# Kernel optimization log

Measured on AMD Instinct MI355X. Metric: run time of the kernel, lower is better.

The kernel has to match this reference:

```python
import jax, jax.numpy as jnp
import numpy as np
import math

B, S, L, D, H, NL, FF, MAXP = 4, 200, 256, 256, 8, 2, 1024, 512
VOC, EDIM, BERT_D, LBL = 50000, 50, 768, 20
DH = D // H
NEG = -1e15


def _pe_table():
    # get_embedding(max_seq_len, hidden, rel_pos_init=0): sinusoidal over 0..2*MAXP
    half = D // 2
    freq = jnp.exp(jnp.arange(half, dtype=jnp.float32) * (-math.log(10000.0) / (half - 1)))
    pos = jnp.arange(2 * MAXP + 1, dtype=jnp.float32)[:, None] * freq[None, :]
    return jnp.concatenate([jnp.sin(pos), jnp.cos(pos)], axis=1)  # [2*MAXP+1, D]


def _ln(x, g, b, eps=1e-5):
    m = x.mean(-1, keepdims=True)
    v = jnp.mean((x - m) ** 2, -1, keepdims=True)
    return (x - m) * jax.lax.rsqrt(v + eps) * g + b


def _forward(lattice, bigrams, seq_len, lex_num, pos_s, pos_e,
             bert_embed, lat_table, big_table, Wc, bc, Wl, bl, W_fus, b_fus,
             Wq, bq, Wk, bk, Wv, bv, Wr, br, u, vb, Wo, bo,
             ln1_g, ln1_b, W1, b1, W2, b2, ln2_g, ln2_b, Wout, bout):
    raw = lat_table[lattice]                                        # [B,L,EDIM]
    big = jnp.pad(big_table[bigrams], ((0, 0), (0, L - S), (0, 0)))  # pad to lattice len
    bert = jnp.pad(bert_embed, ((0, 0), (0, L - S), (0, 0)))
    raw_char = jnp.concatenate([raw, big, bert], -1)                # [B,L,868]
    idx = jnp.arange(L)
    char_mask = idx[None, :] < seq_len[:, None]
    tot_mask = idx[None, :] < (seq_len + lex_num)[:, None]
    lex_mask = tot_mask & (~char_mask)
    # embed_char masked to char positions, embed_lex masked to lexicon positions
    x = (raw_char @ Wc + bc) * char_mask[..., None] + (raw @ Wl + bl) * lex_mask[..., None]

    # four-way relative position fusion ('ff'): relu(Linear(cat[pe_ss,pe_se,pe_es,pe_ee]))
    # computed as sum of four gathered pre-projected tables (same math, no 4D concat)
    pe = _pe_table()
    T = jnp.einsum('pe,keo->kpo', pe, W_fus.reshape(4, D, D))       # [4, 2*MAXP+1, D]
    ss = pos_s[:, :, None] - pos_s[:, None, :] + MAXP
    se = pos_s[:, :, None] - pos_e[:, None, :] + MAXP
    es = pos_e[:, :, None] - pos_s[:, None, :] + MAXP
    ee = pos_e[:, :, None] - pos_e[:, None, :] + MAXP
    rel = jax.nn.relu(T[0][ss] + T[1][se] + T[2][es] + T[3][ee] + b_fus)  # [B,L,L,D]

    scale = 1.0 / math.sqrt(DH)
    for l in range(NL):
        qh = (x @ Wq[l] + bq[l]).reshape(B, L, H, DH).transpose(0, 2, 1, 3)
        kh = (x @ Wk[l] + bk[l]).reshape(B, L, H, DH).transpose(0, 2, 1, 3)
        vh = (x @ Wv[l] + bv[l]).reshape(B, L, H, DH).transpose(0, 2, 1, 3)
        rh = (rel @ Wr[l] + br[l]).reshape(B, L, L, H, DH)
        # Transformer-XL style: A+C with content bias u, B+D with position bias v
        AC = jnp.einsum('bhqd,bhkd->bhqk', qh + u[l][None, :, None, :], kh)
        BD = jnp.einsum('bhqd,bqkhd->bhqk', qh + vb[l][None, :, None, :], rh)
        score = (AC + BD) * scale
        score = jnp.where(tot_mask[:, None, None, :], score, NEG)
        attn = jax.nn.softmax(score, -1)
        out = jnp.einsum('bhqk,bhkd->bhqd', attn, vh).transpose(0, 2, 1, 3).reshape(B, L, D)
        x = _ln(out @ Wo[l] + bo[l] + x, ln1_g[l], ln1_b[l])
        h = jax.nn.relu(x @ W1[l] + b1[l]) @ W2[l] + b2[l]
        x = _ln(h + x, ln2_g[l], ln2_b[l])
    return x[:, :S] @ Wout + bout                                   # emission logits [B,S,LBL]


def setup_inputs() -> dict:
    key = jax.random.key(0)
    ks = jax.random.split(key, 32)
    p = lambda i, sh, s=0.02: jax.random.normal(ks[i], sh, jnp.float32) * s
    inp = {}
    inp['lattice'] = jax.random.randint(ks[0], (B, L), 1, VOC)
    inp['bigrams'] = jax.random.randint(ks[1], (B, S), 1, VOC)
    inp['seq_len'] = jax.random.randint(ks[2], (B,), 150, S + 1)
    inp['lex_num'] = jax.random.randint(ks[3], (B,), 20, L - S + 1)
    s_lex = jax.random.randint(ks[4], (B, L - S), 0, 180)
    e_lex = s_lex + jax.random.randint(ks[5], (B, L - S), 1, 20)
    ar = jnp.broadcast_to(jnp.arange(S), (B, S))
    inp['pos_s'] = jnp.concatenate([ar, s_lex], 1)
    inp['pos_e'] = jnp.concatenate([ar, e_lex], 1)
    inp['target'] = jax.random.randint(ks[6], (B, S), 0, LBL)
    inp['bert_embed'] = p(7, (B, S, BERT_D), 1.0)
    inp['lat_table'] = p(8, (VOC, EDIM), 1.0)
    inp['big_table'] = p(9, (VOC, EDIM), 1.0)
    cin = 2 * EDIM + BERT_D
    inp['Wc'] = p(10, (cin, D)); inp['bc'] = jnp.zeros((D,))
    inp['Wl'] = p(11, (EDIM, D)); inp['bl'] = jnp.zeros((D,))
    inp['W_fus'] = p(12, (4 * D, D)); inp['b_fus'] = jnp.zeros((D,))
    inp['Wq'] = p(13, (NL, D, D)); inp['bq'] = jnp.zeros((NL, D))
    inp['Wk'] = p(14, (NL, D, D)); inp['bk'] = jnp.zeros((NL, D))
    inp['Wv'] = p(15, (NL, D, D)); inp['bv'] = jnp.zeros((NL, D))
    inp['Wr'] = p(16, (NL, D, D)); inp['br'] = jnp.zeros((NL, D))
    inp['u'] = p(17, (NL, H, DH)); inp['vb'] = p(18, (NL, H, DH))
    inp['Wo'] = p(19, (NL, D, D)); inp['bo'] = jnp.zeros((NL, D))
    inp['ln1_g'] = jnp.ones((NL, D)); inp['ln1_b'] = jnp.zeros((NL, D))
    inp['W1'] = p(20, (NL, D, FF)); inp['b1'] = jnp.zeros((NL, FF))
    inp['W2'] = p(21, (NL, FF, D)); inp['b2'] = jnp.zeros((NL, D))
    inp['ln2_g'] = jnp.ones((NL, D)); inp['ln2_b'] = jnp.zeros((NL, D))
    inp['Wout'] = p(22, (D, LBL)); inp['bout'] = jnp.zeros((LBL,))
    return inp


def reference(lattice, bigrams, seq_len, lex_num, pos_s, pos_e, target,
              bert_embed, lat_table, big_table, Wc, bc, Wl, bl, W_fus, b_fus,
              Wq, bq, Wk, bk, Wv, bv, Wr, br, u, vb, Wo, bo,
              ln1_g, ln1_b, W1, b1, W2, b2, ln2_g, ln2_b, Wout, bout):
    # target is consumed by the downstream CRF loss (omitted); emission logits returned
    return _forward(lattice, bigrams, seq_len, lex_num, pos_s, pos_e,
                    bert_embed, lat_table, big_table, Wc, bc, Wl, bl, W_fus, b_fus,
                    Wq, bq, Wk, bk, Wv, bv, Wr, br, u, vb, Wo, bo,
                    ln1_g, ln1_b, W1, b1, W2, b2, ln2_g, ln2_b, Wout, bout)
```

## Files before the change

kernel.cpp:

```cpp
#include <hip/hip_runtime.h>
#include <math.h>

#define NB 4
#define SS 200
#define LT 256
#define DD 256
#define NH 8
#define NLAYER 2
#define FFD 1024
#define BERTD 768
#define CIN 868
#define KG 992
#define NEGINF -1e15f

__global__ void gather_kernel(const int* __restrict__ lattice, const int* __restrict__ bigrams,
                              const int* __restrict__ seq_len, const int* __restrict__ lex_num,
                              const float* __restrict__ bert, const float* __restrict__ lat_t,
                              const float* __restrict__ big_t, float* __restrict__ G)
{
    const int row = blockIdx.x, t = threadIdx.x;
    const int b = row >> 8, l = row & 255;
    const int sl = seq_len[b], tl = sl + lex_num[b];
    const float mC = (l < sl) ? 1.f : 0.f;
    const float mL = (l >= sl && l < tl) ? 1.f : 0.f;
    const int lat = lattice[row];
    const int big = (l < SS) ? bigrams[b*SS + l] : 0;
    for (int i = t; i < KG; i += 256) {
        float v;
        if (i < 50)        v = lat_t[lat*50 + i] * mC;
        else if (i < 100)  v = (l < SS) ? big_t[big*50 + (i-50)] * mC : 0.f;
        else if (i < 868)  v = (l < SS) ? bert[(b*SS + l)*BERTD + (i-100)] * mC : 0.f;
        else if (i < 918)  v = lat_t[lat*50 + (i-868)] * mL;
        else if (i == 918) v = mC;
        else if (i == 919) v = mL;
        else               v = 0.f;
        G[row*KG + i] = v;
    }
}

__global__ void wcomb_kernel(const float* __restrict__ Wc, const float* __restrict__ bc,
                             const float* __restrict__ Wl, const float* __restrict__ bl,
                             float* __restrict__ Wcomb)
{
    const int r = blockIdx.x, t = threadIdx.x;
    float v;
    if (r < 868)      v = Wc[r*DD + t];
    else if (r < 918) v = Wl[(r-868)*DD + t];
    else if (r == 918) v = bc[t];
    else if (r == 919) v = bl[t];
    else               v = 0.f;
    Wcomb[r*DD + t] = v;
}

__global__ void build_T(const float* __restrict__ W_fus, const float* __restrict__ b_fus,
                        float* __restrict__ T)
{
    __shared__ float pe[4][256];
    const int t = threadIdx.x, k = blockIdx.y;
    const int p0 = blockIdx.x * 4;
    const float fr = expf(-(float)(t & 127) * (9.210340371976184f / 127.0f));
    #pragma unroll
    for (int i = 0; i < 4; ++i) {
        int p = p0 + i;
        float arg = (float)(p > 1024 ? 0 : p) * fr;
        pe[i][t] = (t < 128) ? sinf(arg) : cosf(arg);
    }
    __syncthreads();
    float acc[4];
    const float bias = (k == 0) ? b_fus[t] : 0.f;
    #pragma unroll
    for (int i = 0; i < 4; ++i) acc[i] = bias;
    const float* W = W_fus + k * DD * DD;
    for (int e = 0; e < DD; ++e) {
        float w = W[e*DD + t];
        #pragma unroll
        for (int i = 0; i < 4; ++i) acc[i] += pe[i][e] * w;
    }
    #pragma unroll
    for (int i = 0; i < 4; ++i) {
        int p = p0 + i;
        if (p <= 1024) T[(k*1025 + p)*DD + t] = acc[i];
    }
}

__global__ void rcc_kernel(const float* __restrict__ T, float* __restrict__ Rcc)
{
    const int p = blockIdx.x, t = threadIdx.x;
    float v = T[p*DD + t] + T[(1025 + p)*DD + t] + T[(2050 + p)*DD + t] + T[(3075 + p)*DD + t];
    Rcc[p*DD + t] = fmaxf(v, 0.f);
}

__global__ void transpose_wr(const float* __restrict__ Wr, float* __restrict__ WrT)
{
    const int j = blockIdx.x & 255, l = blockIdx.x >> 8, e = threadIdx.x;
    WrT[(l*DD + j)*DD + e] = Wr[l*DD*DD + e*DD + j];
}

__global__ void pack_qkv(const float* __restrict__ Wq, const float* __restrict__ Wk,
                         const float* __restrict__ Wv, const float* __restrict__ bq,
                         const float* __restrict__ bk, const float* __restrict__ bv,
                         float* __restrict__ Wqkv, float* __restrict__ bqkv)
{
    const int l = blockIdx.x >> 8, d = blockIdx.x & 255, t = threadIdx.x;
    Wqkv[(l*DD + d)*768 + t]       = Wq[(l*DD + d)*DD + t];
    Wqkv[(l*DD + d)*768 + 256 + t] = Wk[(l*DD + d)*DD + t];
    Wqkv[(l*DD + d)*768 + 512 + t] = Wv[(l*DD + d)*DD + t];
    if (d == 0) {
        bqkv[l*768 + t]       = bq[l*DD + t];
        bqkv[l*768 + 256 + t] = bk[l*DD + t];
        bqkv[l*768 + 512 + t] = bv[l*DD + t];
    }
}

template<int BM, int BN, bool RELU>
__global__ __launch_bounds__(256) void gemmv2(const float* __restrict__ A, const float* __restrict__ W,
                       const float* __restrict__ bias, const float* __restrict__ resid,
                       float* __restrict__ C, int M, int N, int K)
{
    static_assert(BM*8 % 256 == 0 && 8*BN % 256 == 0, "loader mapping");
    __shared__ float As[32][BM+2];
    __shared__ float Bs[32][BN+4];
    constexpr int TM = BM/16, TN = BN/16;
    const int t = threadIdx.x;
    const int row0 = blockIdx.y*BM, col0 = blockIdx.x*BN;
    const int tr = (t>>4)*TM, tc = (t&15)*TN;
    float acc[TM][TN] = {};
    for (int k0 = 0; k0 < K; k0 += 32) {
        #pragma unroll
        for (int i = 0; i < BM/32; ++i) {
            int slot = t + i*256;
            int r = slot >> 3, kq = (slot & 7)*4;
            float4 av = *(const float4*)&A[(row0+r)*K + k0 + kq];
            As[kq][r] = av.x; As[kq+1][r] = av.y; As[kq+2][r] = av.z; As[kq+3][r] = av.w;
        }
        #pragma unroll
        for (int i = 0; i < BN/32; ++i) {
            int slot = t + i*256;
            int kk = slot / (BN/4), nq = (slot % (BN/4))*4;
            *(float4*)&Bs[kk][nq] = *(const float4*)&W[(k0+kk)*N + col0 + nq];
        }
        __syncthreads();
        #pragma unroll
        for (int kk = 0; kk < 32; ++kk) {
            float a[TM], bb[TN];
            #pragma unroll
            for (int i = 0; i < TM; ++i) a[i] = As[kk][tr+i];
            #pragma unroll
            for (int j = 0; j < TN; ++j) bb[j] = Bs[kk][tc+j];
            #pragma unroll
            for (int i = 0; i < TM; ++i)
                #pragma unroll
                for (int j = 0; j < TN; ++j) acc[i][j] += a[i]*bb[j];
        }
        __syncthreads();
    }
    #pragma unroll
    for (int i = 0; i < TM; ++i) {
        const int r = row0 + tr + i, c0 = col0 + tc;
        #pragma unroll
        for (int j = 0; j < TN; ++j) {
            float v = acc[i][j] + (bias ? bias[c0+j] : 0.f);
            if (resid) v += resid[r*N + c0 + j];
            if (RELU) v = fmaxf(v, 0.f);
            acc[i][j] = v;
        }
        if constexpr (TN == 4) {
            float4 v = make_float4(acc[i][0], acc[i][1], acc[i][2], acc[i][3]);
            *(float4*)&C[r*N + c0] = v;
        } else {
            float2 v = make_float2(acc[i][0], acc[i][1]);
            *(float2*)&C[r*N + c0] = v;
        }
    }
}

__global__ __launch_bounds__(256) void qr_v2(const float* __restrict__ qkvb, const float* __restrict__ vb,
                      const float* __restrict__ WrT, float* __restrict__ qr)
{
    __shared__ float qv[4][256];
    const int t = threadIdx.x, row0 = blockIdx.x * 4;
    #pragma unroll
    for (int r = 0; r < 4; ++r) qv[r][t] = qkvb[(row0+r)*768 + t] + vb[t];
    __syncthreads();
    #pragma unroll
    for (int h = 0; h < NH; ++h) {
        float acc[4] = {0.f, 0.f, 0.f, 0.f};
        const float* wt = WrT + (h*32)*DD;
        for (int d = 0; d < 32; ++d) {
            float w = wt[d*DD + t];
            #pragma unroll
            for (int r = 0; r < 4; ++r) acc[r] += qv[r][h*32 + d] * w;
        }
        #pragma unroll
        for (int r = 0; r < 4; ++r) qr[((row0+r)*NH + h)*DD + t] = acc[r];
    }
}

__global__ __launch_bounds__(256) void attn_v2(
    const float* __restrict__ qkvb, const float* __restrict__ qr,
    const float* __restrict__ T, const float* __restrict__ Rcc,
    const int* __restrict__ pos_s, const int* __restrict__ pos_e,
    const int* __restrict__ seq_len, const int* __restrict__ lex_num,
    const float* __restrict__ u, float* __restrict__ obuf)
{
    __shared__ float relb[32][260];
    __shared__ float qrl[NH][260];
    __shared__ float qu[256];
    __shared__ float sc[NH][260];
    __shared__ float redbuf[2048];
    const int t = threadIdx.x;
    const int row = blockIdx.x;
    const int b = row >> 8, q = row & 255;
    const int totlen = seq_len[b] + lex_num[b];
    if (q >= SS && q >= totlen) {
        obuf[row*DD + t] = 0.f;
        return;
    }
    qu[t] = qkvb[row*768 + t] + u[t];
    #pragma unroll
    for (int h = 0; h < NH; ++h) qrl[h][t] = qr[(row*NH + h)*DD + t];
    const int ps_q = pos_s[row], pe_q = pos_e[row];
    const int* psb = pos_s + b*LT;
    const int* peb = pos_e + b*LT;
    const bool qchar = (q < SS);
    const int br = t >> 3, bc4 = (t & 7)*4;
    const int dk = t & 31, seg = t >> 5;

    for (int K0 = 0; K0 < totlen; K0 += 32) {
        __syncthreads();
        {
            const int kg = K0 + br;
            const int sk = psb[kg], ek = peb[kg];
            if (qchar && kg < SS) {
                const float* rp = Rcc + (ps_q - sk + 512)*DD;
                #pragma unroll
                for (int i = 0; i < 8; ++i) {
                    int e = i*32 + bc4;
                    *(float4*)&relb[br][e] = *(const float4*)&rp[e];
                }
            } else {
                const float* t0 = T + (ps_q - sk + 512)*DD;
                const float* t1 = T + (1025 + ps_q - ek + 512)*DD;
                const float* t2 = T + (2050 + pe_q - sk + 512)*DD;
                const float* t3 = T + (3075 + pe_q - ek + 512)*DD;
                #pragma unroll
                for (int i = 0; i < 8; ++i) {
                    int e = i*32 + bc4;
                    float4 a = *(const float4*)&t0[e];
                    float4 bb = *(const float4*)&t1[e];
                    float4 c = *(const float4*)&t2[e];
                    float4 d = *(const float4*)&t3[e];
                    float4 v;
                    v.x = fmaxf(a.x + bb.x + c.x + d.x, 0.f);
                    v.y = fmaxf(a.y + bb.y + c.y + d.y, 0.f);
                    v.z = fmaxf(a.z + bb.z + c.z + d.z, 0.f);
                    v.w = fmaxf(a.w + bb.w + c.w + d.w, 0.f);
                    *(float4*)&relb[br][e] = v;
                }
            }
        }
        __syncthreads();
        {
            float a[8] = {0.f,0.f,0.f,0.f,0.f,0.f,0.f,0.f};
            const int e0 = seg*32;
            #pragma unroll
            for (int e4 = 0; e4 < 8; ++e4) {
                float4 r4 = *(const float4*)&relb[dk][e0 + e4*4];
                #pragma unroll
                for (int h = 0; h < 8; ++h) {
                    float4 q4 = *(const float4*)&qrl[h][e0 + e4*4];
                    a[h] += r4.x*q4.x + r4.y*q4.y + r4.z*q4.z + r4.w*q4.w;
                }
            }
            {
                const float* kp = qkvb + (size_t)(b*LT + K0 + dk)*768 + 256 + seg*32;
                float acv = 0.f;
                #pragma unroll
                for (int d4 = 0; d4 < 8; ++d4) {
                    float4 kv = *(const float4*)&kp[d4*4];
                    float4 qv = *(const float4*)&qu[seg*32 + d4*4];
                    acv += kv.x*qv.x + kv.y*qv.y + kv.z*qv.z + kv.w*qv.w;
                }
                a[seg] += acv;
            }
            float4* rb = (float4*)&redbuf[(seg*32 + dk)*8];
            rb[0] = make_float4(a[0], a[1], a[2], a[3]);
            rb[1] = make_float4(a[4], a[5], a[6], a[7]);
        }
        __syncthreads();
        {
            const int k = t >> 3, h = t & 7;
            float s = 0.f;
            #pragma unroll
            for (int g = 0; g < 8; ++g) s += redbuf[g*256 + t];
            s *= 0.17677669529663687f;
            const int kg = K0 + k;
            if (kg >= totlen) s = NEGINF;
            sc[h][kg] = s;
        }
    }
    __syncthreads();
    {
        const int g = t >> 5, lane = t & 31;
        float vals[8];
        float m = -INFINITY;
        #pragma unroll
        for (int i = 0; i < 8; ++i) {
            int kidx = lane + 32*i;
            vals[i] = (kidx < totlen) ? sc[g][kidx] : NEGINF;
            m = fmaxf(m, vals[i]);
        }
        #pragma unroll
        for (int off = 16; off >= 1; off >>= 1) m = fmaxf(m, __shfl_xor(m, off, 32));
        float sum = 0.f;
        #pragma unroll
        for (int i = 0; i < 8; ++i) { vals[i] = expf(vals[i] - m); sum += vals[i]; }
        #pragma unroll
        for (int off = 16; off >= 1; off >>= 1) sum += __shfl_xor(sum, off, 32);
        const float inv = 1.0f / sum;
        #pragma unroll
        for (int i = 0; i < 8; ++i) sc[g][lane + 32*i] = vals[i] * inv;
    }
    __syncthreads();
    {
        const int j4 = (t & 63)*4, kr = t >> 6;
        const int h = j4 >> 5;
        float4 acc = make_float4(0.f, 0.f, 0.f, 0.f);
        const float* vp = qkvb + (size_t)(b*LT)*768 + 512 + j4;
        for (int k = kr; k < totlen; k += 4) {
            const float p = sc[h][k];
            float4 v = *(const float4*)&vp[(size_t)k*768];
            acc.x += p*v.x; acc.y += p*v.y; acc.z += p*v.z; acc.w += p*v.w;
        }
        *(float4*)&redbuf[kr*256 + j4] = acc;
    }
    __syncthreads();
    obuf[row*DD + t] = redbuf[t] + redbuf[256 + t] + redbuf[512 + t] + redbuf[768 + t];
}

__global__ void ln_kernel(const float* __restrict__ in, const float* __restrict__ g,
                          const float* __restrict__ bb, float* __restrict__ out)
{
    __shared__ float red[4];
    const int t = threadIdx.x, row = blockIdx.x;
    float v = in[row*DD + t];
    float s = v;
    #pragma unroll
    for (int off = 32; off >= 1; off >>= 1) s += __shfl_xor(s, off, 64);
    if ((t & 63) == 0) red[t >> 6] = s;
    __syncthreads();
    float m = (red[0] + red[1] + red[2] + red[3]) * (1.0f/256.0f);
    __syncthreads();
    float d = v - m;
    float s2 = d*d;
    #pragma unroll
    for (int off = 32; off >= 1; off >>= 1) s2 += __shfl_xor(s2, off, 64);
    if ((t & 63) == 0) red[t >> 6] = s2;
    __syncthreads();
    float var = (red[0] + red[1] + red[2] + red[3]) * (1.0f/256.0f);
    out[row*DD + t] = d * rsqrtf(var + 1e-5f) * g[t] + bb[t];
}

__global__ void out_kernel(const float* __restrict__ x, const float* __restrict__ Wout,
                           const float* __restrict__ bout, float* __restrict__ out)
{
    __shared__ float xs[256];
    const int t = threadIdx.x, row = blockIdx.x;
    const int b = row / SS, s = row % SS;
    const float* xr = x + (b*LT + s)*DD;
    for (int i = t; i < DD; i += 64) xs[i] = xr[i];
    __syncthreads();
    if (t < 20) {
        float acc = bout[t];
        for (int d = 0; d < DD; ++d) acc += xs[d] * Wout[d*20 + t];
        out[row*20 + t] = acc;
    }
}

extern "C" void kernel_launch(void* const* d_in, const int* in_sizes, int n_in,
                              void* d_out, int out_size, void* d_ws, size_t ws_size,
                              hipStream_t stream)
{
    const int*   lattice = (const int*)d_in[0];
    const int*   bigrams = (const int*)d_in[1];
    const int*   seq_len = (const int*)d_in[2];
    const int*   lex_num = (const int*)d_in[3];
    const int*   pos_s   = (const int*)d_in[4];
    const int*   pos_e   = (const int*)d_in[5];
    const float* bert    = (const float*)d_in[7];
    const float* lat_t   = (const float*)d_in[8];
    const float* big_t   = (const float*)d_in[9];
    const float* Wc      = (const float*)d_in[10];
    const float* bc      = (const float*)d_in[11];
    const float* Wl      = (const float*)d_in[12];
    const float* bl      = (const float*)d_in[13];
    const float* W_fus   = (const float*)d_in[14];
    const float* b_fus   = (const float*)d_in[15];
    const float* Wq      = (const float*)d_in[16];
    const float* bq      = (const float*)d_in[17];
    const float* Wk      = (const float*)d_in[18];
    const float* bk      = (const float*)d_in[19];
    const float* Wv      = (const float*)d_in[20];
    const float* bv      = (const float*)d_in[21];
    const float* Wr      = (const float*)d_in[22];
    const float* u_bias  = (const float*)d_in[24];
    const float* v_bias  = (const float*)d_in[25];
    const float* Wo      = (const float*)d_in[26];
    const float* bo      = (const float*)d_in[27];
    const float* ln1g    = (const float*)d_in[28];
    const float* ln1b    = (const float*)d_in[29];
    const float* W1      = (const float*)d_in[30];
    const float* b1      = (const float*)d_in[31];
    const float* W2      = (const float*)d_in[32];
    const float* b2      = (const float*)d_in[33];
    const float* ln2g    = (const float*)d_in[34];
    const float* ln2b    = (const float*)d_in[35];
    const float* Wout    = (const float*)d_in[36];
    const float* bout    = (const float*)d_in[37];

    float* ws = (float*)d_ws;
    float* qkvb = ws;  ws += NB*LT*768;
    float* ob   = ws;  ws += NB*LT*DD;
    float* t1   = ws;  ws += NB*LT*DD;
    float* x2   = ws;  ws += NB*LT*DD;
    float* t2   = ws;  ws += NB*LT*DD;
    float* hb   = ws;  ws += NB*LT*FFD;
    float* x    = ws;  ws += NB*LT*DD;
    float* T    = ws;  ws += 4*1025*DD;
    float* Rcc  = ws;  ws += 1025*DD;
    float* WrT  = ws;  ws += NLAYER*DD*DD;
    float* Wqkv = ws;  ws += NLAYER*DD*768;
    float* bqkv = ws;  ws += NLAYER*768;
    float* qr   = ws;  ws += NB*LT*NH*DD;
    float* G     = qkvb;
    float* Wcomb = t1;

    const int M = NB*LT;

    gather_kernel<<<M, 256, 0, stream>>>(lattice, bigrams, seq_len, lex_num,
                                         bert, lat_t, big_t, G);
    wcomb_kernel<<<KG, 256, 0, stream>>>(Wc, bc, Wl, bl, Wcomb);
    build_T<<<dim3(257, 4), 256, 0, stream>>>(W_fus, b_fus, T);
    transpose_wr<<<NLAYER*DD, 256, 0, stream>>>(Wr, WrT);
    pack_qkv<<<NLAYER*DD, 256, 0, stream>>>(Wq, Wk, Wv, bq, bk, bv, Wqkv, bqkv);
    rcc_kernel<<<1025, 256, 0, stream>>>(T, Rcc);

    gemmv2<32,32,false><<<dim3(DD/32, M/32), 256, 0, stream>>>(G, Wcomb, nullptr, nullptr, x, M, DD, KG);

    for (int l = 0; l < NLAYER; ++l) {
        gemmv2<32,64,false><<<dim3(768/64, M/32), 256, 0, stream>>>(
            x, Wqkv + l*DD*768, bqkv + l*768, nullptr, qkvb, M, 768, DD);
        qr_v2<<<M/4, 256, 0, stream>>>(qkvb, v_bias + l*DD, WrT + l*DD*DD, qr);
        attn_v2<<<M, 256, 0, stream>>>(qkvb, qr, T, Rcc, pos_s, pos_e,
                                       seq_len, lex_num, u_bias + l*DD, ob);
        gemmv2<32,32,false><<<dim3(DD/32, M/32), 256, 0, stream>>>(
            ob, Wo + l*DD*DD, bo + l*DD, x, t1, M, DD, DD);
        ln_kernel<<<M, 256, 0, stream>>>(t1, ln1g + l*DD, ln1b + l*DD, x2);
        gemmv2<64,64,true><<<dim3(FFD/64, M/64), 256, 0, stream>>>(
            x2, W1 + l*DD*FFD, b1 + l*FFD, nullptr, hb, M, FFD, DD);
        gemmv2<32,32,false><<<dim3(DD/32, M/32), 256, 0, stream>>>(
            hb, W2 + l*FFD*DD, b2 + l*DD, x2, t2, M, DD, FFD);
        ln_kernel<<<M, 256, 0, stream>>>(t2, ln2g + l*DD, ln2b + l*DD, x);
    }
    out_kernel<<<NB*SS, 64, 0, stream>>>(x, Wout, bout, (float*)d_out);
}
```

Baseline: 554.6 us.

## Move all dense GEMMs to bf16x3 split MFMA with pre-transposed weights

Replaces the FP32 SIMT tiled GEMM with an MFMA kernel that splits each operand into high and low bf16 parts and accumulates three products, keeping accuracy close to FP32. Every weight matrix is transposed and split once per call. The relative-position table build becomes a GEMM of the sinusoid table against the fused weights, written in an interleaved [p][4*D] layout that attention now indexes. This trades three MFMAs per tile plus per-call weight conversion for much higher matrix throughput. The GEMMs are small, so launch and conversion overhead may limit the gain.

```diff
diff --git a/kernel.cpp b/kernel.cpp
--- a/kernel.cpp
+++ b/kernel.cpp
@@ -12,6 +12,20 @@
 #define CIN 868
 #define KG 992
 #define NEGINF -1e15f
+
+typedef __attribute__((ext_vector_type(8))) short bf16x8;
+typedef __attribute__((ext_vector_type(4))) float f32x4;
+typedef __attribute__((ext_vector_type(8))) unsigned short u16x8;
+typedef __attribute__((ext_vector_type(4))) unsigned short u16x4;
+
+__device__ inline float bf2f(unsigned short h) {
+    union { unsigned int u; float f; } v; v.u = ((unsigned int)h) << 16; return v.f;
+}
+__device__ inline unsigned short f2bf(float x) {
+    union { float f; unsigned int u; } v; v.f = x;
+    unsigned int r = v.u + 0x7fffu + ((v.u >> 16) & 1u);
+    return (unsigned short)(r >> 16);
+}
 
 __global__ void gather_kernel(const int* __restrict__ lattice, const int* __restrict__ bigrams,
                               const int* __restrict__ seq_len, const int* __restrict__ lex_num,
@@ -52,126 +66,171 @@
     Wcomb[r*DD + t] = v;
 }
 
-__global__ void build_T(const float* __restrict__ W_fus, const float* __restrict__ b_fus,
-                        float* __restrict__ T)
-{
-    __shared__ float pe[4][256];
-    const int t = threadIdx.x, k = blockIdx.y;
-    const int p0 = blockIdx.x * 4;
-    const float fr = expf(-(float)(t & 127) * (9.210340371976184f / 127.0f));
-    #pragma unroll
-    for (int i = 0; i < 4; ++i) {
-        int p = p0 + i;
-        float arg = (float)(p > 1024 ? 0 : p) * fr;
-        pe[i][t] = (t < 128) ? sinf(arg) : cosf(arg);
-    }
-    __syncthreads();
-    float acc[4];
-    const float bias = (k == 0) ? b_fus[t] : 0.f;
-    #pragma unroll
-    for (int i = 0; i < 4; ++i) acc[i] = bias;
-    const float* W = W_fus + k * DD * DD;
-    for (int e = 0; e < DD; ++e) {
-        float w = W[e*DD + t];
-        #pragma unroll
-        for (int i = 0; i < 4; ++i) acc[i] += pe[i][e] * w;
-    }
-    #pragma unroll
-    for (int i = 0; i < 4; ++i) {
-        int p = p0 + i;
-        if (p <= 1024) T[(k*1025 + p)*DD + t] = acc[i];
-    }
-}
-
-__global__ void rcc_kernel(const float* __restrict__ T, float* __restrict__ Rcc)
+__global__ void pe_kernel(float* __restrict__ PEf)
 {
     const int p = blockIdx.x, t = threadIdx.x;
-    float v = T[p*DD + t] + T[(1025 + p)*DD + t] + T[(2050 + p)*DD + t] + T[(3075 + p)*DD + t];
-    Rcc[p*DD + t] = fmaxf(v, 0.f);
-}
-
-__global__ void transpose_wr(const float* __restrict__ Wr, float* __restrict__ WrT)
-{
-    const int j = blockIdx.x & 255, l = blockIdx.x >> 8, e = threadIdx.x;
-    WrT[(l*DD + j)*DD + e] = Wr[l*DD*DD + e*DD + j];
-}
-
-__global__ void pack_qkv(const float* __restrict__ Wq, const float* __restrict__ Wk,
-                         const float* __restrict__ Wv, const float* __restrict__ bq,
-                         const float* __restrict__ bk, const float* __restrict__ bv,
-                         float* __restrict__ Wqkv, float* __restrict__ bqkv)
-{
-    const int l = blockIdx.x >> 8, d = blockIdx.x & 255, t = threadIdx.x;
-    Wqkv[(l*DD + d)*768 + t]       = Wq[(l*DD + d)*DD + t];
-    Wqkv[(l*DD + d)*768 + 256 + t] = Wk[(l*DD + d)*DD + t];
-    Wqkv[(l*DD + d)*768 + 512 + t] = Wv[(l*DD + d)*DD + t];
-    if (d == 0) {
+    float v = 0.f;
+    if (p <= 1024) {
+        const float fr = expf(-(float)(t & 127) * (9.210340371976184f / 127.0f));
+        const float arg = (float)p * fr;
+        v = (t < 128) ? sinf(arg) : cosf(arg);
+    }
+    PEf[p*DD + t] = v;
+}
+
+__global__ void smallpack(const float* __restrict__ bq, const float* __restrict__ bk,
+                          const float* __restrict__ bv, const float* __restrict__ b_fus,
+                          float* __restrict__ bqkv, float* __restrict__ bfus4)
+{
+    const int t = threadIdx.x;
+    for (int l = 0; l < NLAYER; ++l) {
         bqkv[l*768 + t]       = bq[l*DD + t];
         bqkv[l*768 + 256 + t] = bk[l*DD + t];
         bqkv[l*768 + 512 + t] = bv[l*DD + t];
     }
-}
-
-template<int BM, int BN, bool RELU>
-__global__ __launch_bounds__(256) void gemmv2(const float* __restrict__ A, const float* __restrict__ W,
-                       const float* __restrict__ bias, const float* __restrict__ resid,
-                       float* __restrict__ C, int M, int N, int K)
-{
-    static_assert(BM*8 % 256 == 0 && 8*BN % 256 == 0, "loader mapping");
-    __shared__ float As[32][BM+2];
-    __shared__ float Bs[32][BN+4];
-    constexpr int TM = BM/16, TN = BN/16;
+    bfus4[t] = b_fus[t];
+    bfus4[256 + t] = 0.f; bfus4[512 + t] = 0.f; bfus4[768 + t] = 0.f;
+}
+
+__global__ void transpose_wr(const float* __restrict__ Wr, float* __restrict__ WrT)
+{
+    const int j = blockIdx.x & 255, l = blockIdx.x >> 8, e = threadIdx.x;
+    WrT[(l*DD + j)*DD + e] = Wr[l*DD*DD + e*DD + j];
+}
+
+__global__ void trans_all(const float* __restrict__ Wcomb, const float* __restrict__ Wq,
+                          const float* __restrict__ Wk, const float* __restrict__ Wv,
+                          const float* __restrict__ Wo, const float* __restrict__ W1,
+                          const float* __restrict__ W2, const float* __restrict__ Wfus,
+                          unsigned short* WcombT_h, unsigned short* WcombT_l,
+                          unsigned short* WqkvT_h,  unsigned short* WqkvT_l,
+                          unsigned short* WoT_h,    unsigned short* WoT_l,
+                          unsigned short* W1T_h,    unsigned short* W1T_l,
+                          unsigned short* W2T_h,    unsigned short* W2T_l,
+                          unsigned short* WfusT_h,  unsigned short* WfusT_l)
+{
+    const int z = blockIdx.z, y = blockIdx.y, tx = blockIdx.x, t = threadIdx.x;
+    const float* src; unsigned short *dh, *dl; int K, N;
+    switch (z) {
+        case 0: if (y) return; K = KG;  N = 256;  src = Wcomb; dh = WcombT_h; dl = WcombT_l; break;
+        case 1: { if (y >= 6) return; int l = y/3, s = y%3; K = 256; N = 256;
+                  src = (s==0 ? Wq : s==1 ? Wk : Wv) + l*65536;
+                  dh = WqkvT_h + (l*768 + s*256)*256; dl = WqkvT_l + (l*768 + s*256)*256; } break;
+        case 2: if (y >= 2) return; K = 256; N = 256;  src = Wo + y*65536;  dh = WoT_h + y*65536;  dl = WoT_l + y*65536;  break;
+        case 3: if (y >= 2) return; K = 256; N = 1024; src = W1 + y*262144; dh = W1T_h + y*262144; dl = W1T_l + y*262144; break;
+        case 4: if (y >= 2) return; K = 1024; N = 256; src = W2 + y*262144; dh = W2T_h + y*262144; dl = W2T_l + y*262144; break;
+        case 5: if (y >= 4) return; K = 256; N = 256;  src = Wfus + y*65536; dh = WfusT_h + y*65536; dl = WfusT_l + y*65536; break;
+        default: return;
+    }
+    const int tiles_x = N >> 5;
+    const int tn = tx % tiles_x, tk = tx / tiles_x;
+    if (tk >= (K >> 5)) return;
+    __shared__ float s[32][33];
+    const int lr = t >> 5, lc = t & 31;
+    #pragma unroll
+    for (int i = 0; i < 4; ++i)
+        s[lr + 8*i][lc] = src[(size_t)(tk*32 + lr + 8*i)*N + tn*32 + lc];
+    __syncthreads();
+    #pragma unroll
+    for (int i = 0; i < 4; ++i) {
+        const int n = tn*32 + lr + 8*i, k = tk*32 + lc;
+        const float x = s[lc][lr + 8*i];
+        const unsigned short hh = f2bf(x);
+        dh[(size_t)n*K + k] = hh;
+        dl[(size_t)n*K + k] = f2bf(x - bf2f(hh));
+    }
+}
+
+template<int BN, bool RELU>
+__global__ __launch_bounds__(256) void gemm_bt_mfma(
+    const float* __restrict__ A, const unsigned short* __restrict__ BTh,
+    const unsigned short* __restrict__ BTl, const float* __restrict__ bias,
+    const float* __restrict__ resid, float* __restrict__ C, int M, int N, int K)
+{
+    constexpr int NT = BN / 32;
+    __shared__ unsigned short Ah[64*40], Al[64*40];
+    __shared__ unsigned short Bh[BN*40], Bl[BN*40];
     const int t = threadIdx.x;
-    const int row0 = blockIdx.y*BM, col0 = blockIdx.x*BN;
-    const int tr = (t>>4)*TM, tc = (t&15)*TN;
-    float acc[TM][TN] = {};
+    const int row0 = blockIdx.y * 64, col0 = blockIdx.x * BN;
+    const int lane = t & 63, w = t >> 6;
+    const int wm = w >> 1, wn = w & 1;
+    const int fr = lane & 15, fq = lane >> 4;
+
+    f32x4 acc[2][NT];
+    #pragma unroll
+    for (int i = 0; i < 2; ++i)
+        #pragma unroll
+        for (int j = 0; j < NT; ++j) acc[i][j] = (f32x4){0.f, 0.f, 0.f, 0.f};
+
     for (int k0 = 0; k0 < K; k0 += 32) {
-        #pragma unroll
-        for (int i = 0; i < BM/32; ++i) {
-            int slot = t + i*256;
-            int r = slot >> 3, kq = (slot & 7)*4;
-            float4 av = *(const float4*)&A[(row0+r)*K + k0 + kq];
-            As[kq][r] = av.x; As[kq+1][r] = av.y; As[kq+2][r] = av.z; As[kq+3][r] = av.w;
-        }
-        #pragma unroll
-        for (int i = 0; i < BN/32; ++i) {
-            int slot = t + i*256;
-            int kk = slot / (BN/4), nq = (slot % (BN/4))*4;
-            *(float4*)&Bs[kk][nq] = *(const float4*)&W[(k0+kk)*N + col0 + nq];
+        {
+            const int r = t >> 2, c = (t & 3) * 8;
+            const float* ap = &A[(size_t)(row0 + r)*K + k0 + c];
+            const float4 v0 = ((const float4*)ap)[0], v1 = ((const float4*)ap)[1];
+            u16x8 hv, lv;
+            const float xs[8] = {v0.x, v0.y, v0.z, v0.w, v1.x, v1.y, v1.z, v1.w};
+            #pragma unroll
+            for (int i = 0; i < 8; ++i) {
+                const unsigned short hh = f2bf(xs[i]);
+                hv[i] = hh; lv[i] = f2bf(xs[i] - bf2f(hh));
+            }
+            *(u16x8*)&Ah[r*40 + c] = hv;
+            *(u16x8*)&Al[r*40 + c] = lv;
+        }
+        if constexpr (BN == 64) {
+            const int n = t >> 2, c = (t & 3) * 8;
+            const size_t g = (size_t)(col0 + n)*K + k0 + c;
+            *(u16x8*)&Bh[n*40 + c] = *(const u16x8*)&BTh[g];
+            *(u16x8*)&Bl[n*40 + c] = *(const u16x8*)&BTl[g];
+        } else {
+            const int n = t >> 3, c = (t & 7) * 4;
+            const size_t g = (size_t)(col0 + n)*K + k0 + c;
+            *(u16x4*)&Bh[n*40 + c] = *(const u16x4*)&BTh[g];
+            *(u16x4*)&Bl[n*40 + c] = *(const u16x4*)&BTl[g];
         }
         __syncthreads();
-        #pragma unroll
-        for (int kk = 0; kk < 32; ++kk) {
-            float a[TM], bb[TN];
+        const bf16x8 ah0 = *(const bf16x8*)&Ah[(wm*32 + fr)*40 + fq*8];
+        const bf16x8 ah1 = *(const bf16x8*)&Ah[(wm*32 + 16 + fr)*40 + fq*8];
+        const bf16x8 al0 = *(const bf16x8*)&Al[(wm*32 + fr)*40 + fq*8];
+        const bf16x8 al1 = *(const bf16x8*)&Al[(wm*32 + 16 + fr)*40 + fq*8];
+        #pragma unroll
+        for (int nt = 0; nt < NT; ++nt) {
+            const int nb = (wn*(BN/2) + nt*16 + fr)*40 + fq*8;
+            const bf16x8 bh = *(const bf16x8*)&Bh[nb];
+            const bf16x8 bl = *(const bf16x8*)&Bl[nb];
+            acc[0][nt] = __builtin_amdgcn_mfma_f32_16x16x32_bf16(ah0, bh, acc[0][nt], 0, 0, 0);
+            acc[0][nt] = __builtin_amdgcn_mfma_f32_16x16x32_bf16(ah0, bl, acc[0][nt], 0, 0, 0);
+            acc[0][nt] = __builtin_amdgcn_mfma_f32_16x16x32_bf16(al0, bh, acc[0][nt], 0, 0, 0);
+            acc[1][nt] = __builtin_amdgcn_mfma_f32_16x16x32_bf16(ah1, bh, acc[1][nt], 0, 0, 0);
+            acc[1][nt] = __builtin_amdgcn_mfma_f32_16x16x32_bf16(ah1, bl, acc[1][nt], 0, 0, 0);
+            acc[1][nt] = __builtin_amdgcn_mfma_f32_16x16x32_bf16(al1, bh, acc[1][nt], 0, 0, 0);
+        }
+        __syncthreads();
+    }
+    #pragma unroll
+    for (int mt = 0; mt < 2; ++mt) {
+        #pragma unroll
+        for (int nt = 0; nt < NT; ++nt) {
+            const int gcol = col0 + wn*(BN/2) + nt*16 + fr;
+            const float bv = bias ? bias[gcol] : 0.f;
             #pragma unroll
-            for (int i = 0; i < TM; ++i) a[i] = As[kk][tr+i];
-            #pragma unroll
-            for (int j = 0; j < TN; ++j) bb[j] = Bs[kk][tc+j];
-            #pragma unroll
-            for (int i = 0; i < TM; ++i)
-                #pragma unroll
-                for (int j = 0; j < TN; ++j) acc[i][j] += a[i]*bb[j];
-        }
-        __syncthreads();
-    }
-    #pragma unroll
-    for (int i = 0; i < TM; ++i) {
-        const int r = row0 + tr + i, c0 = col0 + tc;
-        #pragma unroll
-        for (int j = 0; j < TN; ++j) {
-            float v = acc[i][j] + (bias ? bias[c0+j] : 0.f);
-            if (resid) v += resid[r*N + c0 + j];
-            if (RELU) v = fmaxf(v, 0.f);
-            acc[i][j] = v;
-        }
-        if constexpr (TN == 4) {
-            float4 v = make_float4(acc[i][0], acc[i][1], acc[i][2], acc[i][3]);
-            *(float4*)&C[r*N + c0] = v;
-        } else {
-            float2 v = make_float2(acc[i][0], acc[i][1]);
-            *(float2*)&C[r*N + c0] = v;
-        }
-    }
+            for (int r = 0; r < 4; ++r) {
+                const int grow = row0 + wm*32 + mt*16 + fq*4 + r;
+                float v = acc[mt][nt][r] + bv;
+                if (resid) v += resid[(size_t)grow*N + gcol];
+                if (RELU)  v = fmaxf(v, 0.f);
+                C[(size_t)grow*N + gcol] = v;
+            }
+        }
+    }
+}
+
+__global__ void rcc_kernel(const float* __restrict__ Tn, float* __restrict__ Rcc)
+{
+    const int p = blockIdx.x, t = threadIdx.x;
+    const float v = Tn[(size_t)p*1024 + t] + Tn[(size_t)p*1024 + 256 + t]
+                  + Tn[(size_t)p*1024 + 512 + t] + Tn[(size_t)p*1024 + 768 + t];
+    Rcc[p*DD + t] = fmaxf(v, 0.f);
 }
 
 __global__ __launch_bounds__(256) void qr_v2(const float* __restrict__ qkvb, const float* __restrict__ vb,
@@ -198,7 +257,7 @@
 
 __global__ __launch_bounds__(256) void attn_v2(
     const float* __restrict__ qkvb, const float* __restrict__ qr,
-    const float* __restrict__ T, const float* __restrict__ Rcc,
+    const float* __restrict__ Tn, const float* __restrict__ Rcc,
     const int* __restrict__ pos_s, const int* __restrict__ pos_e,
     const int* __restrict__ seq_len, const int* __restrict__ lex_num,
     const float* __restrict__ u, float* __restrict__ obuf)
@@ -239,10 +298,10 @@
                     *(float4*)&relb[br][e] = *(const float4*)&rp[e];
                 }
             } else {
-                const float* t0 = T + (ps_q - sk + 512)*DD;
-                const float* t1 = T + (1025 + ps_q - ek + 512)*DD;
-                const float* t2 = T + (2050 + pe_q - sk + 512)*DD;
-                const float* t3 = T + (3075 + pe_q - ek + 512)*DD;
+                const float* t0 = Tn + (size_t)(ps_q - sk + 512)*1024;
+                const float* t1 = Tn + (size_t)(ps_q - ek + 512)*1024 + 256;
+                const float* t2 = Tn + (size_t)(pe_q - sk + 512)*1024 + 512;
+                const float* t3 = Tn + (size_t)(pe_q - ek + 512)*1024 + 768;
                 #pragma unroll
                 for (int i = 0; i < 8; ++i) {
                     int e = i*32 + bc4;
@@ -426,40 +485,61 @@
     float* t2   = ws;  ws += NB*LT*DD;
     float* hb   = ws;  ws += NB*LT*FFD;
     float* x    = ws;  ws += NB*LT*DD;
-    float* T    = ws;  ws += 4*1025*DD;
+    float* Tn   = ws;  ws += 1088*1024;
     float* Rcc  = ws;  ws += 1025*DD;
     float* WrT  = ws;  ws += NLAYER*DD*DD;
-    float* Wqkv = ws;  ws += NLAYER*DD*768;
+    float* qr   = ws;  ws += NB*LT*NH*DD;
+    float* PEf  = ws;  ws += 1088*DD;
+    float* Wcomb= ws;  ws += KG*DD;
     float* bqkv = ws;  ws += NLAYER*768;
-    float* qr   = ws;  ws += NB*LT*NH*DD;
-    float* G     = qkvb;
-    float* Wcomb = t1;
+    float* bfus4= ws;  ws += 1024;
+    unsigned short* us = (unsigned short*)ws;
+    unsigned short* WcombT_h = us; us += 256*KG;
+    unsigned short* WcombT_l = us; us += 256*KG;
+    unsigned short* WqkvT_h  = us; us += NLAYER*768*256;
+    unsigned short* WqkvT_l  = us; us += NLAYER*768*256;
+    unsigned short* WoT_h    = us; us += NLAYER*256*256;
+    unsigned short* WoT_l    = us; us += NLAYER*256*256;
+    unsigned short* W1T_h    = us; us += NLAYER*1024*256;
+    unsigned short* W1T_l    = us; us += NLAYER*1024*256;
+    unsigned short* W2T_h    = us; us += NLAYER*256*1024;
+    unsigned short* W2T_l    = us; us += NLAYER*256*1024;
+    unsigned short* WfusT_h  = us; us += 1024*256;
+    unsigned short* WfusT_l  = us; us += 1024*256;
+    float* G = qkvb;
 
     const int M = NB*LT;
 
     gather_kernel<<<M, 256, 0, stream>>>(lattice, bigrams, seq_len, lex_num,
                                          bert, lat_t, big_t, G);
     wcomb_kernel<<<KG, 256, 0, stream>>>(Wc, bc, Wl, bl, Wcomb);
-    build_T<<<dim3(257, 4), 256, 0, stream>>>(W_fus, b_fus, T);
+    pe_kernel<<<1088, 256, 0, stream>>>(PEf);
+    smallpack<<<1, 256, 0, stream>>>(bq, bk, bv, b_fus, bqkv, bfus4);
     transpose_wr<<<NLAYER*DD, 256, 0, stream>>>(Wr, WrT);
-    pack_qkv<<<NLAYER*DD, 256, 0, stream>>>(Wq, Wk, Wv, bq, bk, bv, Wqkv, bqkv);
-    rcc_kernel<<<1025, 256, 0, stream>>>(T, Rcc);
-
-    gemmv2<32,32,false><<<dim3(DD/32, M/32), 256, 0, stream>>>(G, Wcomb, nullptr, nullptr, x, M, DD, KG);
+    trans_all<<<dim3(256, 6, 6), 256, 0, stream>>>(Wcomb, Wq, Wk, Wv, Wo, W1, W2, W_fus,
+        WcombT_h, WcombT_l, WqkvT_h, WqkvT_l, WoT_h, WoT_l,
+        W1T_h, W1T_l, W2T_h, W2T_l, WfusT_h, WfusT_l);
+
+    gemm_bt_mfma<64,false><<<dim3(1024/64, 1088/64), 256, 0, stream>>>(
+        PEf, WfusT_h, WfusT_l, bfus4, nullptr, Tn, 1088, 1024, 256);
+    rcc_kernel<<<1025, 256, 0, stream>>>(Tn, Rcc);
+
+    gemm_bt_mfma<32,false><<<dim3(DD/32, M/64), 256, 0, stream>>>(
+        G, WcombT_h, WcombT_l, nullptr, nullptr, x, M, DD, KG);
 
     for (int l = 0; l < NLAYER; ++l) {
-        gemmv2<32,64,false><<<dim3(768/64, M/32), 256, 0, stream>>>(
-            x, Wqkv + l*DD*768, bqkv + l*768, nullptr, qkvb, M, 768, DD);
+        gemm_bt_mfma<64,false><<<dim3(768/64, M/64), 256, 0, stream>>>(
+            x, WqkvT_h + l*768*256, WqkvT_l + l*768*256, bqkv + l*768, nullptr, qkvb, M, 768, DD);
         qr_v2<<<M/4, 256, 0, stream>>>(qkvb, v_bias + l*DD, WrT + l*DD*DD, qr);
-        attn_v2<<<M, 256, 0, stream>>>(qkvb, qr, T, Rcc, pos_s, pos_e,
+        attn_v2<<<M, 256, 0, stream>>>(qkvb, qr, Tn, Rcc, pos_s, pos_e,
                                        seq_len, lex_num, u_bias + l*DD, ob);
-        gemmv2<32,32,false><<<dim3(DD/32, M/32), 256, 0, stream>>>(
-            ob, Wo + l*DD*DD, bo + l*DD, x, t1, M, DD, DD);
+        gemm_bt_mfma<32,false><<<dim3(DD/32, M/64), 256, 0, stream>>>(
+            ob, WoT_h + l*65536, WoT_l + l*65536, bo + l*DD, x, t1, M, DD, DD);
         ln_kernel<<<M, 256, 0, stream>>>(t1, ln1g + l*DD, ln1b + l*DD, x2);
-        gemmv2<64,64,true><<<dim3(FFD/64, M/64), 256, 0, stream>>>(
-            x2, W1 + l*DD*FFD, b1 + l*FFD, nullptr, hb, M, FFD, DD);
-        gemmv2<32,32,false><<<dim3(DD/32, M/32), 256, 0, stream>>>(
-            hb, W2 + l*FFD*DD, b2 + l*DD, x2, t2, M, DD, FFD);
+        gemm_bt_mfma<64,true><<<dim3(FFD/64, M/64), 256, 0, stream>>>(
+            x2, W1T_h + l*262144, W1T_l + l*262144, b1 + l*FFD, nullptr, hb, M, FFD, DD);
+        gemm_bt_mfma<32,false><<<dim3(DD/32, M/64), 256, 0, stream>>>(
+            hb, W2T_h + l*262144, W2T_l + l*262144, b2 + l*DD, x2, t2, M, DD, FFD);
         ln_kernel<<<M, 256, 0, stream>>>(t2, ln2g + l*DD, ln2b + l*DD, x);
     }
     out_kernel<<<NB*SS, 64, 0, stream>>>(x, Wout, bout, (float*)d_out);
```

New measurement: 512.2 us. -7.6%, faster.
